# Kernel optimization log

Hardware: AMD Instinct MI355X
Metric: run time of the kernel (lower is better)

## Reference

```python
import jax, jax.numpy as jnp
import numpy as np

IN_FEATURE = 256
OUT_FEATURE = 128
ALPHA = 0.5  # LeakyReLU negative slope
NEG_BIG = -9e15


def setup_inputs() -> dict:
    key = jax.random.key(0)
    k1, k2, k3, k4 = jax.random.split(key, 4)
    N = 8192
    x = jax.random.normal(k1, (N, IN_FEATURE), dtype=jnp.float32)
    adj = jax.random.randint(k2, (N, N), 0, 2, dtype=jnp.int32)
    stdv = 1.0 / np.sqrt(OUT_FEATURE)
    W = jax.random.uniform(k3, (IN_FEATURE, OUT_FEATURE), dtype=jnp.float32,
                           minval=-stdv, maxval=stdv)
    a = jax.random.uniform(k4, (2 * OUT_FEATURE, 1), dtype=jnp.float32,
                           minval=-stdv, maxval=stdv)
    return {"input": x, "adj": adj, "W": W, "a": a}


def reference(input, adj, W, a):
    # h: [N, F_out]
    h = input @ W
    # Additive attention: cat([h_i, h_j]) @ a == h_i @ a1 + h_j @ a2
    a1 = a[:OUT_FEATURE, 0]   # [F_out]
    a2 = a[OUT_FEATURE:, 0]   # [F_out]
    f1 = h @ a1               # [N]  (row / source contribution)
    f2 = h @ a2               # [N]  (col / target contribution)
    e = jax.nn.leaky_relu(f1[:, None] + f2[None, :], negative_slope=ALPHA)  # [N, N]
    scores = jnp.where(adj > 0, e, NEG_BIG)
    attention = jax.nn.softmax(scores, axis=1)  # [N, N]
    h_prime = attention @ h                     # [N, F_out]
    return jax.nn.elu(h_prime)
```

## Files before the change

kernel.cpp:

```cpp
#include <hip/hip_runtime.h>

#define N_NODES 8192
#define IN_F 256
#define OUT_F 128
#define ALPHA 0.5f
#define JC 8
#define KCHUNK 1024
#define ROUNDS 32

using short8 = __attribute__((ext_vector_type(8))) short;
using f32x4  = __attribute__((ext_vector_type(4))) float;

__device__ __forceinline__ unsigned int f2bf(float f){
  unsigned int u = __float_as_uint(f);
  u += 0x7fffu + ((u >> 16) & 1u);
  return u >> 16;
}

__global__ __launch_bounds__(256) void k_h(const float* __restrict__ x,
                                           const float* __restrict__ W,
                                           float* __restrict__ h){
  __shared__ float xs[16*IN_F];
  const int tid = threadIdx.x;
  const int r0 = blockIdx.x * 16;
  const float4* xg = (const float4*)(x + (size_t)r0*IN_F);
  float4* xl = (float4*)xs;
  #pragma unroll
  for(int i=0;i<4;i++) xl[tid + i*256] = xg[tid + i*256];
  __syncthreads();
  const int wave = tid >> 6, lane = tid & 63;
  float2 acc[4];
  #pragma unroll
  for(int j=0;j<4;j++){ acc[j].x = 0.f; acc[j].y = 0.f; }
  const float2* Wp = (const float2*)W;
  for(int k4=0;k4<IN_F;k4+=4){
    float4 xq[4];
    #pragma unroll
    for(int j=0;j<4;j++) xq[j] = *(const float4*)&xs[(wave*4+j)*IN_F + k4];
    #pragma unroll
    for(int kk=0;kk<4;kk++){
      float2 wv = Wp[(size_t)(k4+kk)*64 + lane];
      #pragma unroll
      for(int j=0;j<4;j++){
        float xv = kk==0?xq[j].x : kk==1?xq[j].y : kk==2?xq[j].z : xq[j].w;
        acc[j].x += xv*wv.x; acc[j].y += xv*wv.y;
      }
    }
  }
  #pragma unroll
  for(int j=0;j<4;j++)
    *(float2*)(h + (size_t)(r0 + wave*4 + j)*OUT_F + lane*2) = acc[j];
}

__global__ __launch_bounds__(256) void k_f(const float* __restrict__ h,
                                           const float* __restrict__ a,
                                           float* __restrict__ f1,
                                           float* __restrict__ f2){
  const int wave = threadIdx.x >> 6, lane = threadIdx.x & 63;
  const int row = blockIdx.x*4 + wave;
  float2 hv = ((const float2*)(h + (size_t)row*OUT_F))[lane];
  float2 a1 = ((const float2*)a)[lane];
  float2 a2 = ((const float2*)(a + OUT_F))[lane];
  float s1 = hv.x*a1.x + hv.y*a1.y;
  float s2 = hv.x*a2.x + hv.y*a2.y;
  #pragma unroll
  for(int off=32; off; off>>=1){
    s1 += __shfl_down(s1, off);
    s2 += __shfl_down(s2, off);
  }
  if(lane == 0){ f1[row] = s1; f2[row] = s2; }
}

#define LDW 132
__global__ __launch_bounds__(256) void k_pack(const float* __restrict__ h,
                                              unsigned short* __restrict__ P){
  __shared__ float ld[32*LDW];
  const int tid = threadIdx.x;
  const int kb = blockIdx.x, j0 = kb*32;
  #pragma unroll
  for(int i=0;i<4;i++){
    int idx = tid + i*256;
    int row = idx >> 5, c4 = (idx & 31)*4;
    *(float4*)&ld[row*LDW + c4] = *(const float4*)(h + (size_t)(j0+row)*OUT_F + c4);
  }
  __syncthreads();
  #pragma unroll
  for(int i=0;i<2;i++){
    int o = tid*2 + i;
    int c = o >> 6, lane = o & 63;
    int q = lane >> 4, n = lane & 15;
    short8 v;
    #pragma unroll
    for(int t=0;t<8;t++) v[t] = (short)f2bf(ld[(q*8+t)*LDW + c*16 + n]);
    *(short8*)(P + ((size_t)(kb*8 + c)*64 + lane)*8) = v;
  }
}

__global__ __launch_bounds__(256) void k_comp(const int* __restrict__ adj,
                                              unsigned long long* __restrict__ bm){
  const int lane = threadIdx.x & 63;
  const int wid = (blockIdx.x*256 + threadIdx.x) >> 6;
  const int nw = (gridDim.x*256) >> 6;
  const size_t total = (size_t)N_NODES*N_NODES;
  for(size_t base = (size_t)wid*512; base < total; base += (size_t)nw*512){
    unsigned long long msk[8];
    #pragma unroll
    for(int u=0;u<8;u++){
      int v = adj[base + (size_t)u*64 + lane];
      msk[u] = __ballot(v > 0);
    }
    if(lane < 8){
      unsigned long long v = msk[0];
      #pragma unroll
      for(int u=1;u<8;u++) v = (lane == u) ? msk[u] : v;
      bm[base/64 + lane] = v;
    }
  }
}

__global__ __launch_bounds__(256, 2) void k_attn(
    const unsigned int* __restrict__ bmw,
    const unsigned short* __restrict__ P,
    const float* __restrict__ f1, const float* __restrict__ f2,
    float* __restrict__ part, float* __restrict__ denp){
  __shared__ unsigned int bs[128*32];
  __shared__ float f2s[KCHUNK];
  __shared__ float f1s[128];
  const int tid = threadIdx.x;
  const int wave = tid >> 6, lane = tid & 63;
  const int m = lane & 15, q = lane >> 4;
  const int jc = blockIdx.x;
  const int r0b = blockIdx.y * 128;

  ((float4*)f2s)[tid] = ((const float4*)(f2 + jc*KCHUNK))[tid];
  if(tid < 128) f1s[tid] = f1[r0b + tid];
  {
    const int row = tid >> 1, h16 = (tid & 1) * 16;
    const unsigned int* src = bmw + (size_t)(r0b + row)*256 + jc*32 + h16;
    const int sw = row & 31;
    #pragma unroll
    for(int i=0;i<16;i+=4){
      uint4 v = *(const uint4*)(src + i);
      bs[row*32 + ((h16+i  ) ^ sw)] = v.x;
      bs[row*32 + ((h16+i+1) ^ sw)] = v.y;
      bs[row*32 + ((h16+i+2) ^ sw)] = v.z;
      bs[row*32 + ((h16+i+3) ^ sw)] = v.w;
    }
  }
  __syncthreads();

  const int rg0 = wave*32 + m;
  const float rf1a = f1s[rg0], rf1b = f1s[rg0 + 16];
  const unsigned int* bw0 = &bs[rg0*32];
  const unsigned int* bw1 = &bs[(rg0+16)*32];
  const int x0 = rg0 & 31, x1 = (rg0+16) & 31;
  const short8* PB = (const short8*)P + (size_t)jc*ROUNDS*512 + lane;

  f32x4 acc0[8], acc1[8];
  #pragma unroll
  for(int c=0;c<8;c++){ acc0[c] = (f32x4){0,0,0,0}; acc1[c] = (f32x4){0,0,0,0}; }
  float den0 = 0.f, den1 = 0.f;

  auto wcalc = [&](unsigned int bits, float4 fa, float4 fb,
                   float rf1, float& den) -> short8 {
    short8 af; float t, w;
    #define WE(slot, fv)                                  \
      t = rf1 + (fv); t = fmaxf(t, ALPHA*t);              \
      w = (bits & (1u<<(slot))) ? __expf(t) : 0.f;        \
      den += w; af[slot] = (short)f2bf(w);
    WE(0,fa.x) WE(1,fa.y) WE(2,fa.z) WE(3,fa.w)
    WE(4,fb.x) WE(5,fb.y) WE(6,fb.z) WE(7,fb.w)
    #undef WE
    return af;
  };

  short8 Bf[8], Bn[8];
  #pragma unroll
  for(int c=0;c<8;c++) Bn[c] = PB[c*64];

  for(int rd=0; rd<ROUNDS; rd++){
    #pragma unroll
    for(int c=0;c<8;c++) Bf[c] = Bn[c];
    if(rd+1 < ROUNDS){
      const short8* Bq = PB + (size_t)(rd+1)*512;
      #pragma unroll
      for(int c=0;c<8;c++) Bn[c] = Bq[c*64];
    }
    unsigned int b0 = (bw0[rd ^ x0] >> (q*8)) & 0xffu;
    unsigned int b1 = (bw1[rd ^ x1] >> (q*8)) & 0xffu;
    float4 fva = *(const float4*)(f2s + rd*32 + q*8);
    float4 fvb = *(const float4*)(f2s + rd*32 + q*8 + 4);
    short8 af0 = wcalc(b0, fva, fvb, rf1a, den0);
    short8 af1 = wcalc(b1, fva, fvb, rf1b, den1);
    #pragma unroll
    for(int c=0;c<8;c++){
      acc0[c] = __builtin_amdgcn_mfma_f32_16x16x32_bf16(af0, Bf[c], acc0[c], 0,0,0);
      acc1[c] = __builtin_amdgcn_mfma_f32_16x16x32_bf16(af1, Bf[c], acc1[c], 0,0,0);
    }
  }

  den0 += __shfl_down(den0, 32); den0 += __shfl_down(den0, 16);
  den1 += __shfl_down(den1, 32); den1 += __shfl_down(den1, 16);
  const int r0w = r0b + wave*32;
  if(lane < 16){
    denp[(size_t)jc*N_NODES + r0w + lane]      = den0;
    denp[(size_t)jc*N_NODES + r0w + 16 + lane] = den1;
  }
  float* pp = part + (size_t)jc*N_NODES*OUT_F;
  #pragma unroll
  for(int c=0;c<8;c++){
    #pragma unroll
    for(int reg=0;reg<4;reg++){
      pp[(size_t)(r0w + q*4 + reg)*OUT_F      + c*16 + m] = acc0[c][reg];
      pp[(size_t)(r0w + 16 + q*4 + reg)*OUT_F + c*16 + m] = acc1[c][reg];
    }
  }
}

__global__ __launch_bounds__(256) void k_out(const float* __restrict__ part,
    const float* __restrict__ denp, float* __restrict__ out){
  const int idx = blockIdx.x*256 + threadIdx.x;
  const int r = idx >> 7;
  float v = 0.f, d = 0.f;
  #pragma unroll
  for(int p=0;p<JC;p++){
    v += part[(size_t)p*N_NODES*OUT_F + idx];
    d += denp[(size_t)p*N_NODES + r];
  }
  v /= d;
  out[idx] = v > 0.f ? v : (__expf(v) - 1.f);
}

extern "C" void kernel_launch(void* const* d_in, const int* in_sizes, int n_in,
                              void* d_out, int out_size, void* d_ws, size_t ws_size,
                              hipStream_t stream){
  const float* x   = (const float*)d_in[0];
  const int*   adj = (const int*)d_in[1];
  const float* W   = (const float*)d_in[2];
  const float* a   = (const float*)d_in[3];
  char* ws = (char*)d_ws;
  float* h            = (float*)ws;
  unsigned short* P   = (unsigned short*)(ws + (4u<<20));
  float* f1           = (float*)(ws + (6u<<20));
  float* f2           = (float*)(ws + (6u<<20) + (32u<<10));
  float* part         = (float*)(ws + (8u<<20));
  float* denp         = (float*)(ws + (40u<<20));
  unsigned long long* bm = (unsigned long long*)(ws + (48u<<20));
  float* out          = (float*)d_out;

  k_comp<<<2048, 256, 0, stream>>>(adj, bm);
  k_h<<<512, 256, 0, stream>>>(x, W, h);
  k_f<<<2048, 256, 0, stream>>>(h, a, f1, f2);
  k_pack<<<256, 256, 0, stream>>>(h, P);
  k_attn<<<dim3(JC,64), 256, 0, stream>>>((const unsigned int*)bm, P, f1, f2, part, denp);
  k_out<<<(N_NODES*OUT_F)/256, 256, 0, stream>>>(part, denp, out);
}
```

Baseline: 441.0 us.

## Fuse h/f/pack kernels and stage attention B tiles through LDS

```diff
diff --git a/kernel.cpp b/kernel.cpp
--- a/kernel.cpp
+++ b/kernel.cpp
@@ -17,82 +17,79 @@
   return u >> 16;
 }
 
-__global__ __launch_bounds__(256) void k_h(const float* __restrict__ x,
-                                           const float* __restrict__ W,
-                                           float* __restrict__ h){
-  __shared__ float xs[16*IN_F];
+__global__ __launch_bounds__(256) void k_hfp(const float* __restrict__ x,
+                                             const float* __restrict__ W,
+                                             const float* __restrict__ a,
+                                             float* __restrict__ f1,
+                                             float* __restrict__ f2,
+                                             unsigned short* __restrict__ P){
+  __shared__ float xs[32*IN_F];
+  __shared__ unsigned short hl[32*136];
   const int tid = threadIdx.x;
-  const int r0 = blockIdx.x * 16;
+  const int r0 = blockIdx.x * 32;
   const float4* xg = (const float4*)(x + (size_t)r0*IN_F);
-  float4* xl = (float4*)xs;
-  #pragma unroll
-  for(int i=0;i<4;i++) xl[tid + i*256] = xg[tid + i*256];
+  #pragma unroll
+  for(int i=0;i<8;i++) ((float4*)xs)[tid + i*256] = xg[tid + i*256];
   __syncthreads();
   const int wave = tid >> 6, lane = tid & 63;
-  float2 acc[4];
-  #pragma unroll
-  for(int j=0;j<4;j++){ acc[j].x = 0.f; acc[j].y = 0.f; }
+  float2 acc[8];
+  #pragma unroll
+  for(int j=0;j<8;j++){ acc[j].x = 0.f; acc[j].y = 0.f; }
   const float2* Wp = (const float2*)W;
   for(int k4=0;k4<IN_F;k4+=4){
-    float4 xq[4];
-    #pragma unroll
-    for(int j=0;j<4;j++) xq[j] = *(const float4*)&xs[(wave*4+j)*IN_F + k4];
+    float4 xq[8];
+    #pragma unroll
+    for(int j=0;j<8;j++) xq[j] = *(const float4*)&xs[(wave*8+j)*IN_F + k4];
     #pragma unroll
     for(int kk=0;kk<4;kk++){
       float2 wv = Wp[(size_t)(k4+kk)*64 + lane];
       #pragma unroll
-      for(int j=0;j<4;j++){
+      for(int j=0;j<8;j++){
         float xv = kk==0?xq[j].x : kk==1?xq[j].y : kk==2?xq[j].z : xq[j].w;
         acc[j].x += xv*wv.x; acc[j].y += xv*wv.y;
       }
     }
   }
-  #pragma unroll
-  for(int j=0;j<4;j++)
-    *(float2*)(h + (size_t)(r0 + wave*4 + j)*OUT_F + lane*2) = acc[j];
-}
-
-__global__ __launch_bounds__(256) void k_f(const float* __restrict__ h,
-                                           const float* __restrict__ a,
-                                           float* __restrict__ f1,
-                                           float* __restrict__ f2){
-  const int wave = threadIdx.x >> 6, lane = threadIdx.x & 63;
-  const int row = blockIdx.x*4 + wave;
-  float2 hv = ((const float2*)(h + (size_t)row*OUT_F))[lane];
-  float2 a1 = ((const float2*)a)[lane];
-  float2 a2 = ((const float2*)(a + OUT_F))[lane];
-  float s1 = hv.x*a1.x + hv.y*a1.y;
-  float s2 = hv.x*a2.x + hv.y*a2.y;
-  #pragma unroll
-  for(int off=32; off; off>>=1){
-    s1 += __shfl_down(s1, off);
-    s2 += __shfl_down(s2, off);
-  }
-  if(lane == 0){ f1[row] = s1; f2[row] = s2; }
-}
-
-#define LDW 132
-__global__ __launch_bounds__(256) void k_pack(const float* __restrict__ h,
-                                              unsigned short* __restrict__ P){
-  __shared__ float ld[32*LDW];
-  const int tid = threadIdx.x;
-  const int kb = blockIdx.x, j0 = kb*32;
-  #pragma unroll
-  for(int i=0;i<4;i++){
-    int idx = tid + i*256;
-    int row = idx >> 5, c4 = (idx & 31)*4;
-    *(float4*)&ld[row*LDW + c4] = *(const float4*)(h + (size_t)(j0+row)*OUT_F + c4);
+  {
+    float2 a1 = ((const float2*)a)[lane];
+    float2 a2 = ((const float2*)(a + OUT_F))[lane];
+    float s1[8], s2[8];
+    #pragma unroll
+    for(int j=0;j<8;j++){
+      s1[j] = acc[j].x*a1.x + acc[j].y*a1.y;
+      s2[j] = acc[j].x*a2.x + acc[j].y*a2.y;
+    }
+    #pragma unroll
+    for(int off=32; off; off>>=1){
+      #pragma unroll
+      for(int j=0;j<8;j++){
+        s1[j] += __shfl_down(s1[j], off);
+        s2[j] += __shfl_down(s2[j], off);
+      }
+    }
+    if(lane == 0){
+      #pragma unroll
+      for(int j=0;j<8;j++){
+        f1[r0 + wave*8 + j] = s1[j];
+        f2[r0 + wave*8 + j] = s2[j];
+      }
+    }
+  }
+  #pragma unroll
+  for(int j=0;j<8;j++){
+    unsigned int u = f2bf(acc[j].x) | (f2bf(acc[j].y) << 16);
+    *(unsigned int*)&hl[(wave*8+j)*136 + 2*lane] = u;
   }
   __syncthreads();
   #pragma unroll
   for(int i=0;i<2;i++){
     int o = tid*2 + i;
-    int c = o >> 6, lane = o & 63;
-    int q = lane >> 4, n = lane & 15;
+    int c = o >> 6, ln = o & 63;
+    int q = ln >> 4, n = ln & 15;
     short8 v;
     #pragma unroll
-    for(int t=0;t<8;t++) v[t] = (short)f2bf(ld[(q*8+t)*LDW + c*16 + n]);
-    *(short8*)(P + ((size_t)(kb*8 + c)*64 + lane)*8) = v;
+    for(int t=0;t<8;t++) v[t] = (short)hl[(q*8+t)*136 + c*16 + n];
+    *(short8*)(P + ((size_t)(blockIdx.x*8 + c)*64 + ln)*8) = v;
   }
 }
 
@@ -126,6 +123,7 @@
   __shared__ unsigned int bs[128*32];
   __shared__ float f2s[KCHUNK];
   __shared__ float f1s[128];
+  __shared__ __align__(16) short Bst[2][4096];
   const int tid = threadIdx.x;
   const int wave = tid >> 6, lane = tid & 63;
   const int m = lane & 15, q = lane >> 4;
@@ -147,64 +145,72 @@
       bs[row*32 + ((h16+i+3) ^ sw)] = v.w;
     }
   }
-  __syncthreads();
 
   const int rg0 = wave*32 + m;
-  const float rf1a = f1s[rg0], rf1b = f1s[rg0 + 16];
   const unsigned int* bw0 = &bs[rg0*32];
   const unsigned int* bw1 = &bs[(rg0+16)*32];
   const int x0 = rg0 & 31, x1 = (rg0+16) & 31;
-  const short8* PB = (const short8*)P + (size_t)jc*ROUNDS*512 + lane;
-
-  f32x4 acc0[8], acc1[8];
+  const short8* PB = (const short8*)P + (size_t)jc*ROUNDS*512;
+  const int sl0 = (2*wave)*64 + lane, sl1 = sl0 + 64;
+
+  f32x4 acc0[8], acc1[8], accd0 = {0,0,0,0}, accd1 = {0,0,0,0};
   #pragma unroll
   for(int c=0;c<8;c++){ acc0[c] = (f32x4){0,0,0,0}; acc1[c] = (f32x4){0,0,0,0}; }
-  float den0 = 0.f, den1 = 0.f;
-
-  auto wcalc = [&](unsigned int bits, float4 fa, float4 fb,
-                   float rf1, float& den) -> short8 {
-    short8 af; float t, w;
-    #define WE(slot, fv)                                  \
-      t = rf1 + (fv); t = fmaxf(t, ALPHA*t);              \
-      w = (bits & (1u<<(slot))) ? __expf(t) : 0.f;        \
-      den += w; af[slot] = (short)f2bf(w);
+  const short8 ones = {0x3F80,0x3F80,0x3F80,0x3F80,0x3F80,0x3F80,0x3F80,0x3F80};
+
+  short8 Bp0 = PB[sl0], Bp1 = PB[sl1];
+  __syncthreads();
+  const float rf1a = f1s[rg0], rf1b = f1s[rg0 + 16];
+
+  auto wc8 = [&](unsigned int bits, float4 fa, float4 fb, float rf1) -> short8 {
+    float w[8]; float t;
+    #define WE(i, fv)                                      \
+      t = rf1 + (fv); t = fmaxf(t, ALPHA*t);               \
+      w[i] = (bits & (1u<<(i))) ? __expf(t) : 0.f;
     WE(0,fa.x) WE(1,fa.y) WE(2,fa.z) WE(3,fa.w)
     WE(4,fb.x) WE(5,fb.y) WE(6,fb.z) WE(7,fb.w)
     #undef WE
-    return af;
+    union { short8 s; uint4 u; } r;
+    #pragma unroll
+    for(int i=0;i<4;i++)
+      r.u[i] = __builtin_amdgcn_perm(__float_as_uint(w[2*i+1]),
+                                     __float_as_uint(w[2*i]), 0x07060302);
+    return r.s;
   };
 
-  short8 Bf[8], Bn[8];
-  #pragma unroll
-  for(int c=0;c<8;c++) Bn[c] = PB[c*64];
-
   for(int rd=0; rd<ROUNDS; rd++){
-    #pragma unroll
-    for(int c=0;c<8;c++) Bf[c] = Bn[c];
+    short8* Bw = (short8*)Bst[rd & 1];
+    Bw[sl0] = Bp0; Bw[sl1] = Bp1;
+    __syncthreads();
     if(rd+1 < ROUNDS){
-      const short8* Bq = PB + (size_t)(rd+1)*512;
-      #pragma unroll
-      for(int c=0;c<8;c++) Bn[c] = Bq[c*64];
+      Bp0 = PB[(rd+1)*512 + sl0];
+      Bp1 = PB[(rd+1)*512 + sl1];
     }
     unsigned int b0 = (bw0[rd ^ x0] >> (q*8)) & 0xffu;
     unsigned int b1 = (bw1[rd ^ x1] >> (q*8)) & 0xffu;
     float4 fva = *(const float4*)(f2s + rd*32 + q*8);
     float4 fvb = *(const float4*)(f2s + rd*32 + q*8 + 4);
-    short8 af0 = wcalc(b0, fva, fvb, rf1a, den0);
-    short8 af1 = wcalc(b1, fva, fvb, rf1b, den1);
+    short8 af0 = wc8(b0, fva, fvb, rf1a);
+    short8 af1 = wc8(b1, fva, fvb, rf1b);
+    const short8* Br = (const short8*)Bst[rd & 1] + lane;
     #pragma unroll
     for(int c=0;c<8;c++){
-      acc0[c] = __builtin_amdgcn_mfma_f32_16x16x32_bf16(af0, Bf[c], acc0[c], 0,0,0);
-      acc1[c] = __builtin_amdgcn_mfma_f32_16x16x32_bf16(af1, Bf[c], acc1[c], 0,0,0);
-    }
-  }
-
-  den0 += __shfl_down(den0, 32); den0 += __shfl_down(den0, 16);
-  den1 += __shfl_down(den1, 32); den1 += __shfl_down(den1, 16);
+      short8 Bf = Br[c*64];
+      acc0[c] = __builtin_amdgcn_mfma_f32_16x16x32_bf16(af0, Bf, acc0[c], 0,0,0);
+      acc1[c] = __builtin_amdgcn_mfma_f32_16x16x32_bf16(af1, Bf, acc1[c], 0,0,0);
+    }
+    accd0 = __builtin_amdgcn_mfma_f32_16x16x32_bf16(af0, ones, accd0, 0,0,0);
+    accd1 = __builtin_amdgcn_mfma_f32_16x16x32_bf16(af1, ones, accd1, 0,0,0);
+    __syncthreads();
+  }
+
   const int r0w = r0b + wave*32;
-  if(lane < 16){
-    denp[(size_t)jc*N_NODES + r0w + lane]      = den0;
-    denp[(size_t)jc*N_NODES + r0w + 16 + lane] = den1;
+  if(m == 0){
+    #pragma unroll
+    for(int reg=0;reg<4;reg++){
+      denp[(size_t)jc*N_NODES + r0w + q*4 + reg]      = accd0[reg];
+      denp[(size_t)jc*N_NODES + r0w + 16 + q*4 + reg] = accd1[reg];
+    }
   }
   float* pp = part + (size_t)jc*N_NODES*OUT_F;
   #pragma unroll
@@ -239,7 +245,6 @@
   const float* W   = (const float*)d_in[2];
   const float* a   = (const float*)d_in[3];
   char* ws = (char*)d_ws;
-  float* h            = (float*)ws;
   unsigned short* P   = (unsigned short*)(ws + (4u<<20));
   float* f1           = (float*)(ws + (6u<<20));
   float* f2           = (float*)(ws + (6u<<20) + (32u<<10));
@@ -249,9 +254,7 @@
   float* out          = (float*)d_out;
 
   k_comp<<<2048, 256, 0, stream>>>(adj, bm);
-  k_h<<<512, 256, 0, stream>>>(x, W, h);
-  k_f<<<2048, 256, 0, stream>>>(h, a, f1, f2);
-  k_pack<<<256, 256, 0, stream>>>(h, P);
+  k_hfp<<<256, 256, 0, stream>>>(x, W, a, f1, f2, P);
   k_attn<<<dim3(JC,64), 256, 0, stream>>>((const unsigned int*)bm, P, f1, f2, part, denp);
   k_out<<<(N_NODES*OUT_F)/256, 256, 0, stream>>>(part, denp, out);
 }
```

Result: no change. 446.0 us (+1.1%).
